# Performance work log

Measured on AMD Instinct MI355X. Metric: run time of the kernel, lower is better.

## Reference

```python
import jax, jax.numpy as jnp
import numpy as np

CH = 512
GROUPS = 32
EPS = 1e-5
B, H, W = 4, 64, 64


def setup_inputs() -> dict:
    key = jax.random.key(0)
    ks = jax.random.split(key, 6)
    s = 1.0 / np.sqrt(CH)  # conv2d default init scale (approx, uniform fan-in)
    return {
        "x": jax.random.normal(ks[0], (B, CH, H, W), dtype=jnp.float32),
        "norm_w": jnp.ones((CH,), jnp.float32),
        "norm_b": jnp.zeros((CH,), jnp.float32),
        "q_w": jax.random.normal(ks[1], (CH, CH), jnp.float32) * s,
        "q_b": jnp.zeros((CH,), jnp.float32),
        "k_w": jax.random.normal(ks[2], (CH, CH), jnp.float32) * s,
        "k_b": jnp.zeros((CH,), jnp.float32),
        "v_w": jax.random.normal(ks[3], (CH, CH), jnp.float32) * s,
        "v_b": jnp.zeros((CH,), jnp.float32),
        "proj_w": jax.random.normal(ks[4], (CH, CH), jnp.float32) * s,
        "proj_b": jnp.zeros((CH,), jnp.float32),
    }


def _group_norm(x, w, b):
    # x: [B, C, H, W]; 32 groups over channel dim
    bsz, c, h, wd = x.shape
    xg = x.reshape(bsz, GROUPS, c // GROUPS, h, wd)
    mean = xg.mean(axis=(2, 3, 4), keepdims=True)
    var = xg.var(axis=(2, 3, 4), keepdims=True)
    xg = (xg - mean) * jax.lax.rsqrt(var + EPS)
    x = xg.reshape(bsz, c, h, wd)
    return x * w[None, :, None, None] + b[None, :, None, None]


def _conv1x1(x, w, b):
    # x: [B, C, H, W], w: [O, C] -> [B, O, H, W]
    return jnp.einsum('bchw,oc->bohw', x, w) + b[None, :, None, None]


def reference(x, norm_w, norm_b, q_w, q_b, k_w, k_b, v_w, v_b, proj_w, proj_b):
    h = _group_norm(x, norm_w, norm_b)
    b, c, hh, ww = h.shape
    n = hh * ww
    q = _conv1x1(h, q_w, q_b).reshape(b, c, n).transpose(0, 2, 1)  # [b, n, c]
    k = _conv1x1(h, k_w, k_b).reshape(b, c, n)                     # [b, c, n]
    v = _conv1x1(h, v_w, v_b).reshape(b, c, n).transpose(0, 2, 1)  # [b, n, c]
    attn = jnp.einsum('bnc,bcm->bnm', q, k) * (c ** -0.5)          # [b, n, n]
    attn = jax.nn.softmax(attn, axis=-1)
    out = jnp.einsum('bnm,bmc->bnc', attn, v)                      # [b, n, c]
    out = out.transpose(0, 2, 1).reshape(b, c, hh, ww)
    return x + _conv1x1(out, proj_w, proj_b)
```

## Files before the change

kernel.cpp:

```cpp
#include <hip/hip_runtime.h>

#define NB 4
#define CH 512
#define NPIX 4096
#define GSZ 16
#define KVB 32
#define NT (NPIX / KVB)
#define DYN_LDS 136192
#define GEMM_LDS 65536

typedef __attribute__((ext_vector_type(8))) short bf16x8;
typedef __attribute__((ext_vector_type(4))) short bf16x4;
typedef __attribute__((ext_vector_type(4))) float f32x4;

#define MFMA __builtin_amdgcn_mfma_f32_16x16x32_bf16

static __device__ __forceinline__ short f2bf(float f) {
  unsigned u = __builtin_bit_cast(unsigned, f);
  u += 0x7fffu + ((u >> 16) & 1u);
  return (short)(u >> 16);
}

static __device__ __forceinline__ float bperm_f(int srclane, float v) {
  int r = __builtin_amdgcn_ds_bpermute(srclane << 2, __builtin_bit_cast(int, v));
  return __builtin_bit_cast(float, r);
}

typedef __attribute__((address_space(1))) unsigned glob_u32;
typedef __attribute__((address_space(3))) unsigned lds_u32;
static __device__ __forceinline__ void gl_lds16(const void* g, void* l) {
  __builtin_amdgcn_global_load_lds((const glob_u32*)g, (lds_u32*)l, 16, 0, 0);
}

__global__ __launch_bounds__(256) void wconv_kernel(
    const float* __restrict__ qw, const float* __restrict__ kw,
    const float* __restrict__ vw, const float* __restrict__ pw,
    short* __restrict__ wstack, short* __restrict__ wp) {
  int idx = (blockIdx.x * 256 + threadIdx.x) * 4;
  int mat = idx >> 18;
  int off = idx & 262143;
  const float* src = (mat == 0) ? qw : (mat == 1) ? kw : (mat == 2) ? vw : pw;
  short* dst = (mat < 3) ? (wstack + (size_t)mat * 262144) : wp;
  float4 v = *reinterpret_cast<const float4*>(src + off);
  bf16x4 o;
  o[0] = f2bf(v.x); o[1] = f2bf(v.y); o[2] = f2bf(v.z); o[3] = f2bf(v.w);
  *reinterpret_cast<bf16x4*>(dst + off) = o;
}

__global__ __launch_bounds__(256) void gn_stats_kernel(
    const float* __restrict__ x, float* __restrict__ st) {
  int b = blockIdx.x >> 5, g = blockIdx.x & 31;
  int tid = threadIdx.x;
  const float4* b4 = reinterpret_cast<const float4*>(
      x + (size_t)(b * CH + g * GSZ) * NPIX);
  float s = 0.f, s2 = 0.f;
  for (int i = tid; i < GSZ * NPIX / 4; i += 256) {
    float4 v = b4[i];
    s += v.x + v.y + v.z + v.w;
    s2 += v.x * v.x + v.y * v.y + v.z * v.z + v.w * v.w;
  }
  #pragma unroll
  for (int m = 1; m < 64; m <<= 1) { s += __shfl_xor(s, m); s2 += __shfl_xor(s2, m); }
  __shared__ float red[8];
  if ((tid & 63) == 0) { red[(tid >> 6) * 2] = s; red[(tid >> 6) * 2 + 1] = s2; }
  __syncthreads();
  if (tid == 0) {
    s = red[0] + red[2] + red[4] + red[6];
    s2 = red[1] + red[3] + red[5] + red[7];
    float mean = s * (1.f / 65536.f);
    float var = s2 * (1.f / 65536.f) - mean * mean;
    st[blockIdx.x * 2] = mean;
    st[blockIdx.x * 2 + 1] = rsqrtf(var + 1e-5f);
  }
}

__global__ __launch_bounds__(256) void gn_apply_kernel(
    const float* __restrict__ x, const float* __restrict__ nw,
    const float* __restrict__ nb, const float* __restrict__ st,
    short* __restrict__ hT) {
  int quarter = blockIdx.x & 3, pairid = blockIdx.x >> 2;
  int b = pairid >> 5, g = pairid & 31;
  int tid = threadIdx.x;
  float mean = st[pairid * 2], rstd = st[pairid * 2 + 1];
  int c = tid >> 4, nq = tid & 15;
  float wch = nw[g * GSZ + c] * rstd;
  float bch = nb[g * GSZ + c] - mean * wch;
  __shared__ short lt[GSZ][264];
  const float* base = x + (size_t)(b * CH + g * GSZ) * NPIX;
  short* outb = hT + (size_t)b * NPIX * CH + g * GSZ;
  const float* srcc = base + (size_t)c * NPIX + nq * 16;
  for (int chunk = quarter * 4; chunk < quarter * 4 + 4; ++chunk) {
    const float4* sp = reinterpret_cast<const float4*>(srcc + chunk * 256);
    float4 v0 = sp[0], v1 = sp[1], v2 = sp[2], v3 = sp[3];
    bf16x8 w0, w1;
    w0[0] = f2bf(v0.x * wch + bch); w0[1] = f2bf(v0.y * wch + bch);
    w0[2] = f2bf(v0.z * wch + bch); w0[3] = f2bf(v0.w * wch + bch);
    w0[4] = f2bf(v1.x * wch + bch); w0[5] = f2bf(v1.y * wch + bch);
    w0[6] = f2bf(v1.z * wch + bch); w0[7] = f2bf(v1.w * wch + bch);
    w1[0] = f2bf(v2.x * wch + bch); w1[1] = f2bf(v2.y * wch + bch);
    w1[2] = f2bf(v2.z * wch + bch); w1[3] = f2bf(v2.w * wch + bch);
    w1[4] = f2bf(v3.x * wch + bch); w1[5] = f2bf(v3.y * wch + bch);
    w1[6] = f2bf(v3.z * wch + bch); w1[7] = f2bf(v3.w * wch + bch);
    *reinterpret_cast<bf16x8*>(&lt[c][nq * 16]) = w0;
    *reinterpret_cast<bf16x8*>(&lt[c][nq * 16 + 8]) = w1;
    __syncthreads();
    bf16x8 o0, o1;
    #pragma unroll
    for (int cc = 0; cc < 8; ++cc) o0[cc] = lt[cc][tid];
    #pragma unroll
    for (int cc = 0; cc < 8; ++cc) o1[cc] = lt[cc + 8][tid];
    short* orow = outb + (size_t)(chunk * 256 + tid) * CH;
    *reinterpret_cast<bf16x8*>(orow) = o0;
    *reinterpret_cast<bf16x8*>(orow + 8) = o1;
    __syncthreads();
  }
}

__global__ __launch_bounds__(256) void qkv_kernel(
    const short* __restrict__ wstack, const short* __restrict__ hT,
    const float* __restrict__ qb, const float* __restrict__ kb,
    const float* __restrict__ vb,
    short* __restrict__ qT, short* __restrict__ kT, short* __restrict__ vC) {
  extern __shared__ char qsm[];
  char* abuf = qsm;
  char* bbuf = qsm + 32768;

  int hwid = blockIdx.x;
  int xcd = hwid & 7, slot = hwid >> 3;
  int by = slot % 12, gq = slot / 12;
  int grp = xcd + 8 * gq;
  int b = grp >> 5;
  int nbase = (grp & 31) * 128;
  int tid = threadIdx.x;
  int lane = tid & 63, wid = tid >> 6;
  int l15 = lane & 15, lg = lane >> 4;
  int wr = wid >> 1, wc = wid & 1;

  const short* arows = wstack + (size_t)by * 128 * CH;
  const short* brows = hT + ((size_t)b * NPIX + nbase) * CH;

  auto stage = [&](int buf, int kidx) {
    char* ad = abuf + buf * 16384;
    char* bd = bbuf + buf * 16384;
    #pragma unroll
    for (int i = 0; i < 4; ++i) {
      int off = i * 4096 + tid * 16;
      int row = off >> 7;
      int c16 = (off >> 4) & 7;
      int gchunk = (c16 ^ (row & 7)) * 8;
      gl_lds16(arows + (size_t)row * CH + kidx * 64 + gchunk, ad + off);
      gl_lds16(brows + (size_t)row * CH + kidx * 64 + gchunk, bd + off);
    }
  };

  f32x4 acc[4][4];
  #pragma unroll
  for (int mi = 0; mi < 4; ++mi)
    #pragma unroll
    for (int ni = 0; ni < 4; ++ni) acc[mi][ni] = (f32x4){0.f, 0.f, 0.f, 0.f};

  stage(0, 0);
  __syncthreads();

  int cur = 0;
  for (int kt = 0; kt < 8; ++kt) {
    if (kt + 1 < 8) stage(cur ^ 1, kt + 1);
    const char* ab = abuf + cur * 16384;
    const char* bb = bbuf + cur * 16384;
    #pragma unroll
    for (int ks = 0; ks < 2; ++ks) {
      bf16x8 af[4], bf[4];
      #pragma unroll
      for (int mi = 0; mi < 4; ++mi) {
        int row = wr * 64 + mi * 16 + l15;
        af[mi] = *reinterpret_cast<const bf16x8*>(
            ab + row * 128 + (((ks * 4 + lg) ^ (row & 7)) << 4));
      }
      #pragma unroll
      for (int ni = 0; ni < 4; ++ni) {
        int row = wc * 64 + ni * 16 + l15;
        bf[ni] = *reinterpret_cast<const bf16x8*>(
            bb + row * 128 + (((ks * 4 + lg) ^ (row & 7)) << 4));
      }
      #pragma unroll
      for (int mi = 0; mi < 4; ++mi)
        #pragma unroll
        for (int ni = 0; ni < 4; ++ni)
          acc[mi][ni] = MFMA(af[mi], bf[ni], acc[mi][ni], 0, 0, 0);
    }
    __syncthreads();
    cur ^= 1;
  }

  int oglob = by * 128;
  #pragma unroll
  for (int mi = 0; mi < 4; ++mi) {
    int oo = oglob + wr * 64 + mi * 16 + lg * 4;
    #pragma unroll
    for (int ni = 0; ni < 4; ++ni) {
      int nn = nbase + wc * 64 + ni * 16 + l15;
      f32x4 a = acc[mi][ni];
      if (oglob < 1024) {
        const float* bias = (oglob < 512) ? qb : kb;
        short* dstm = (oglob < 512) ? qT : kT;
        float sc = (oglob < 512) ? 0.044194173824159216f : 1.0f;
        int ol = oo & 511;
        bf16x4 pk;
        #pragma unroll
        for (int r = 0; r < 4; ++r) pk[r] = f2bf((a[r] + bias[ol + r]) * sc);
        *reinterpret_cast<bf16x4*>(dstm + ((size_t)b * NPIX + nn) * CH + ol) = pk;
      } else {
        int ov = oo - 1024;
        short* dstv = vC + ((size_t)b * CH + ov) * NPIX + nn;
        #pragma unroll
        for (int r = 0; r < 4; ++r) dstv[(size_t)r * NPIX] = f2bf(a[r] + vb[ov + r]);
      }
    }
  }
}

__global__ __launch_bounds__(512, 2) void flash_kernel(
    const short* __restrict__ qT, const short* __restrict__ kT,
    const short* __restrict__ vC, short* __restrict__ ao) {
  extern __shared__ char smem[];
  char* kbuf = smem;
  char* vbuf = smem + 65536;
  char* pbuf = smem + 131072;
  float* exch = (float*)(smem + 135168);

  int lin = blockIdx.y * 64 + blockIdx.x;
  int sw = (lin & 7) * 32 + (lin >> 3);
  int qb = sw & 63, b = sw >> 6;

  int tid = threadIdx.x;
  int lane = tid & 63, w = tid >> 6;
  int p = w >> 1, h = w & 1;
  int l15 = lane & 15, lg = lane >> 4;
  int qrow = qb * 64 + p * 16;

  const short* qptr = qT + ((size_t)b * NPIX + qrow + l15) * CH + lg * 8;
  bf16x8 qf[16];
  #pragma unroll
  for (int ks = 0; ks < 16; ++ks) qf[ks] = *reinterpret_cast<const bf16x8*>(qptr + ks * 32);

  f32x4 oacc[16];
  #pragma unroll
  for (int i = 0; i < 16; ++i) oacc[i] = (f32x4){0.f, 0.f, 0.f, 0.f};
  float mrow = -INFINITY, lrow = 0.f;
  bf16x8 pa_prev;
  bf16x8 vf_prev[16];
  #pragma unroll
  for (int i = 0; i < 8; ++i) pa_prev[i] = 0;
  #pragma unroll
  for (int j = 0; j < 16; ++j)
    #pragma unroll
    for (int i = 0; i < 8; ++i) vf_prev[j][i] = 0;

  const short* kTb = kT + (size_t)b * NPIX * CH;
  const short* vCb = vC + (size_t)b * CH * NPIX;
  const int swz = (l15 & 7) << 4;
  const int vswz = ((l15 >> 1) & 3) << 4;
  const int pswz = (l15 & 3) << 4;
  char* ppair = pbuf + p * 1024;
  float* exw = exch + (w * 16 + l15) * 2;
  float* exr = exch + ((w ^ 1) * 16 + l15) * 2;

  auto stage = [&](int buf, int t) {
    int m0 = t * KVB;
    char* kd = kbuf + buf * 32768;
    char* vd = vbuf + buf * 32768;
    #pragma unroll
    for (int i = 0; i < 4; ++i) {
      int r = w * 4 + i;
      const short* src = kTb + (size_t)(m0 + r) * CH + ((lane ^ (r & 7)) * 8);
      gl_lds16(src, kd + r * 1024);
    }
    #pragma unroll
    for (int i = 0; i < 4; ++i) {
      int j = w * 4 + i;
      int ch = j * 16 + (lane >> 2);
      const short* src = vCb + (size_t)ch * NPIX + m0 +
                         (((lane & 3) ^ ((lane >> 3) & 3)) * 8);
      gl_lds16(src, vd + j * 1024);
    }
  };

  stage(0, 0);
  asm volatile("s_waitcnt vmcnt(0)" ::: "memory");
  __syncthreads();

  int cur = 0;
  for (int t = 0; t < NT; ++t) {
    const char* kb_ = kbuf + cur * 32768;
    const char* vb_ = vbuf + cur * 32768;
    if (t + 1 < NT) stage(cur ^ 1, t + 1);
    f32x4 sa = (f32x4){0.f, 0.f, 0.f, 0.f};
    f32x4 sb = (f32x4){0.f, 0.f, 0.f, 0.f};
    __builtin_amdgcn_s_setprio(1);
    #pragma unroll
    for (int cs = 0; cs < 16; cs += 2) {
      bf16x8 kf0 = *reinterpret_cast<const bf16x8*>(
          kb_ + (h * 16 + l15) * 1024 + ((cs * 64 + lg * 16) ^ swz));
      bf16x8 kf1 = *reinterpret_cast<const bf16x8*>(
          kb_ + (h * 16 + l15) * 1024 + (((cs + 1) * 64 + lg * 16) ^ swz));
      sa = MFMA(kf0, qf[cs], sa, 0, 0, 0);
      sb = MFMA(kf1, qf[cs + 1], sb, 0, 0, 0);
    }
    __builtin_amdgcn_s_setprio(0);
    f32x4 st = sa + sb;
    float tmax = fmaxf(fmaxf(st[0], st[1]), fmaxf(st[2], st[3]));
    tmax = fmaxf(tmax, __shfl_xor(tmax, 16));
    tmax = fmaxf(tmax, __shfl_xor(tmax, 32));
    float pr[4];
    float psh;
    pr[0] = __expf(st[0] - tmax); pr[1] = __expf(st[1] - tmax);
    pr[2] = __expf(st[2] - tmax); pr[3] = __expf(st[3] - tmax);
    psh = (pr[0] + pr[1]) + (pr[2] + pr[3]);
    psh += __shfl_xor(psh, 16);
    psh += __shfl_xor(psh, 32);
    if (lane < 16) { exw[0] = tmax; exw[1] = psh; }
    asm volatile("s_waitcnt lgkmcnt(0)" ::: "memory");
    __builtin_amdgcn_s_barrier();
    __builtin_amdgcn_sched_barrier(0);
    float mo = exr[0], po = exr[1];
    float mnew = fmaxf(mrow, fmaxf(tmax, mo));
    float alpha = __expf(mrow - mnew);
    float scl = __expf(tmax - mnew);
    lrow = lrow * alpha + psh * scl + po * __expf(mo - mnew);
    mrow = mnew;
    {
      bf16x4 pk;
      pk[0] = f2bf(pr[0] * scl); pk[1] = f2bf(pr[1] * scl);
      pk[2] = f2bf(pr[2] * scl); pk[3] = f2bf(pr[3] * scl);
      *reinterpret_cast<bf16x4*>(ppair + l15 * 64 + ((h * 32 + lg * 8) ^ pswz)) = pk;
    }
    __builtin_amdgcn_s_setprio(1);
    #pragma unroll
    for (int j = 0; j < 16; ++j)
      oacc[j] = MFMA(pa_prev, vf_prev[j], oacc[j], 0, 0, 0);
    __builtin_amdgcn_s_setprio(0);
    if (!__all(alpha == 1.0f)) {
      float a4[4];
      #pragma unroll
      for (int r = 0; r < 4; ++r) a4[r] = bperm_f(lg * 4 + r, alpha);
      #pragma unroll
      for (int j = 0; j < 16; ++j) {
        oacc[j][0] *= a4[0]; oacc[j][1] *= a4[1];
        oacc[j][2] *= a4[2]; oacc[j][3] *= a4[3];
      }
    }
    #pragma unroll
    for (int j = 0; j < 16; ++j)
      vf_prev[j] = *reinterpret_cast<const bf16x8*>(
          vb_ + ((h * 16 + j) * 16 + l15) * 64 + ((lg * 16) ^ vswz));
    asm volatile("s_waitcnt vmcnt(0) lgkmcnt(0)" ::: "memory");
    __builtin_amdgcn_s_barrier();
    __builtin_amdgcn_sched_barrier(0);
    pa_prev = *reinterpret_cast<const bf16x8*>(ppair + l15 * 64 + ((lg * 16) ^ pswz));
    cur ^= 1;
  }
  #pragma unroll
  for (int j = 0; j < 16; ++j)
    oacc[j] = MFMA(pa_prev, vf_prev[j], oacc[j], 0, 0, 0);

  float linv = 1.f / lrow;
  float r4[4];
  #pragma unroll
  for (int r = 0; r < 4; ++r) r4[r] = bperm_f(lg * 4 + r, linv);
  short* aob = ao + ((size_t)b * NPIX + qrow) * CH;
  #pragma unroll
  for (int j = 0; j < 16; ++j) {
    int cb2 = h * 16 + j;
    #pragma unroll
    for (int r = 0; r < 4; ++r) {
      aob[(size_t)(lg * 4 + r) * CH + cb2 * 16 + l15] = f2bf(oacc[j][r] * r4[r]);
    }
  }
}

__global__ __launch_bounds__(256) void proj_kernel(
    const short* __restrict__ wpm, const short* __restrict__ ao,
    const float* __restrict__ x, const float* __restrict__ pb,
    float* __restrict__ out) {
  extern __shared__ char qsm[];
  char* abuf = qsm;
  char* bbuf = qsm + 32768;

  int hwid = blockIdx.x;
  int xcd = hwid & 7, slot = hwid >> 3;
  int by = slot & 3, gq = slot >> 2;
  int grp = xcd + 8 * gq;
  int b = grp >> 5;
  int nbase = (grp & 31) * 128;
  int tid = threadIdx.x;
  int lane = tid & 63, wid = tid >> 6;
  int l15 = lane & 15, lg = lane >> 4;
  int wr = wid >> 1, wc = wid & 1;

  const short* arows = wpm + (size_t)by * 128 * CH;
  const short* brows = ao + ((size_t)b * NPIX + nbase) * CH;

  auto stage = [&](int buf, int kidx) {
    char* ad = abuf + buf * 16384;
    char* bd = bbuf + buf * 16384;
    #pragma unroll
    for (int i = 0; i < 4; ++i) {
      int off = i * 4096 + tid * 16;
      int row = off >> 7;
      int c16 = (off >> 4) & 7;
      int gchunk = (c16 ^ (row & 7)) * 8;
      gl_lds16(arows + (size_t)row * CH + kidx * 64 + gchunk, ad + off);
      gl_lds16(brows + (size_t)row * CH + kidx * 64 + gchunk, bd + off);
    }
  };

  f32x4 acc[4][4];
  #pragma unroll
  for (int mi = 0; mi < 4; ++mi)
    #pragma unroll
    for (int ni = 0; ni < 4; ++ni) acc[mi][ni] = (f32x4){0.f, 0.f, 0.f, 0.f};

  stage(0, 0);
  __syncthreads();

  int cur = 0;
  for (int kt = 0; kt < 8; ++kt) {
    if (kt + 1 < 8) stage(cur ^ 1, kt + 1);
    const char* ab = abuf + cur * 16384;
    const char* bb = bbuf + cur * 16384;
    #pragma unroll
    for (int ks = 0; ks < 2; ++ks) {
      bf16x8 af[4], bf[4];
      #pragma unroll
      for (int mi = 0; mi < 4; ++mi) {
        int row = wr * 64 + mi * 16 + l15;
        af[mi] = *reinterpret_cast<const bf16x8*>(
            ab + row * 128 + (((ks * 4 + lg) ^ (row & 7)) << 4));
      }
      #pragma unroll
      for (int ni = 0; ni < 4; ++ni) {
        int row = wc * 64 + ni * 16 + l15;
        bf[ni] = *reinterpret_cast<const bf16x8*>(
            bb + row * 128 + (((ks * 4 + lg) ^ (row & 7)) << 4));
      }
      #pragma unroll
      for (int mi = 0; mi < 4; ++mi)
        #pragma unroll
        for (int ni = 0; ni < 4; ++ni)
          acc[mi][ni] = MFMA(af[mi], bf[ni], acc[mi][ni], 0, 0, 0);
    }
    __syncthreads();
    cur ^= 1;
  }

  #pragma unroll
  for (int mi = 0; mi < 4; ++mi) {
    int oo = by * 128 + wr * 64 + mi * 16 + lg * 4;
    #pragma unroll
    for (int ni = 0; ni < 4; ++ni) {
      int nn = nbase + wc * 64 + ni * 16 + l15;
      f32x4 a = acc[mi][ni];
      #pragma unroll
      for (int r = 0; r < 4; ++r) {
        size_t idx = ((size_t)b * CH + oo + r) * NPIX + nn;
        out[idx] = a[r] + pb[oo + r] + x[idx];
      }
    }
  }
}

extern "C" void kernel_launch(void* const* d_in, const int* in_sizes, int n_in,
                              void* d_out, int out_size, void* d_ws, size_t ws_size,
                              hipStream_t stream) {
  const float* x  = (const float*)d_in[0];
  const float* nw = (const float*)d_in[1];
  const float* nb = (const float*)d_in[2];
  const float* qw = (const float*)d_in[3];
  const float* qb = (const float*)d_in[4];
  const float* kw = (const float*)d_in[5];
  const float* kb = (const float*)d_in[6];
  const float* vw = (const float*)d_in[7];
  const float* vb = (const float*)d_in[8];
  const float* pw = (const float*)d_in[9];
  const float* pb = (const float*)d_in[10];
  char* ws = (char*)d_ws;
  short* wstack = (short*)(ws);
  short* wp     = (short*)(ws + 1572864);
  float* gnstat = (float*)(ws + 2097152);
  short* hT     = (short*)(ws + 2101248);
  short* qT     = (short*)(ws + 18878464);
  short* kT     = (short*)(ws + 35655680);
  short* vC     = (short*)(ws + 52432896);
  short* ao     = hT;
  float* out = (float*)d_out;

  hipFuncSetAttribute((const void*)flash_kernel,
                      hipFuncAttributeMaxDynamicSharedMemorySize, DYN_LDS);
  hipFuncSetAttribute((const void*)qkv_kernel,
                      hipFuncAttributeMaxDynamicSharedMemorySize, GEMM_LDS);
  hipFuncSetAttribute((const void*)proj_kernel,
                      hipFuncAttributeMaxDynamicSharedMemorySize, GEMM_LDS);

  wconv_kernel<<<1024, 256, 0, stream>>>(qw, kw, vw, pw, wstack, wp);
  gn_stats_kernel<<<128, 256, 0, stream>>>(x, gnstat);
  gn_apply_kernel<<<512, 256, 0, stream>>>(x, nw, nb, gnstat, hT);
  qkv_kernel<<<1536, 256, GEMM_LDS, stream>>>(wstack, hT, qb, kb, vb, qT, kT, vC);
  flash_kernel<<<dim3(64, NB), 512, DYN_LDS, stream>>>(qT, kT, vC, ao);
  proj_kernel<<<512, 256, GEMM_LDS, stream>>>(wp, ao, x, pb, out);
}
```

Baseline: 435.2 us.

## Double-buffer softmax stats exchange to drop one barrier per KV tile

The two half-waves that split each KV tile now write their row max, row sum and unscaled bf16 probabilities into alternating LDS slots. The cross-half merge of softmax statistics, the rescale of the output accumulators and the rescale of P all move after the existing end-of-iteration barrier. This removes the separate mid-iteration barrier and LDS wait that used to sit between the QK^T and PV phases. In exchange, P is rounded to bf16 twice, slightly reducing precision, and LDS use grows a little.

```diff
diff --git a/kernel.cpp b/kernel.cpp
--- a/kernel.cpp
+++ b/kernel.cpp
@@ -6,7 +6,7 @@
 #define GSZ 16
 #define KVB 32
 #define NT (NPIX / KVB)
-#define DYN_LDS 136192
+#define DYN_LDS 141312
 #define GEMM_LDS 65536
 
 typedef __attribute__((ext_vector_type(8))) short bf16x8;
@@ -19,6 +19,11 @@
   unsigned u = __builtin_bit_cast(unsigned, f);
   u += 0x7fffu + ((u >> 16) & 1u);
   return (short)(u >> 16);
+}
+
+static __device__ __forceinline__ float bf2f(short s) {
+  unsigned u = ((unsigned)(unsigned short)s) << 16;
+  return __builtin_bit_cast(float, u);
 }
 
 static __device__ __forceinline__ float bperm_f(int srclane, float v) {
@@ -226,7 +231,7 @@
   char* kbuf = smem;
   char* vbuf = smem + 65536;
   char* pbuf = smem + 131072;
-  float* exch = (float*)(smem + 135168);
+  float* exch = (float*)(smem + 139264);
 
   int lin = blockIdx.y * 64 + blockIdx.x;
   int sw = (lin & 7) * 32 + (lin >> 3);
@@ -293,6 +298,7 @@
   for (int t = 0; t < NT; ++t) {
     const char* kb_ = kbuf + cur * 32768;
     const char* vb_ = vbuf + cur * 32768;
+    int slot = t & 1;
     if (t + 1 < NT) stage(cur ^ 1, t + 1);
     f32x4 sa = (f32x4){0.f, 0.f, 0.f, 0.f};
     f32x4 sb = (f32x4){0.f, 0.f, 0.f, 0.f};
@@ -318,37 +324,19 @@
     psh = (pr[0] + pr[1]) + (pr[2] + pr[3]);
     psh += __shfl_xor(psh, 16);
     psh += __shfl_xor(psh, 32);
-    if (lane < 16) { exw[0] = tmax; exw[1] = psh; }
-    asm volatile("s_waitcnt lgkmcnt(0)" ::: "memory");
-    __builtin_amdgcn_s_barrier();
-    __builtin_amdgcn_sched_barrier(0);
-    float mo = exr[0], po = exr[1];
-    float mnew = fmaxf(mrow, fmaxf(tmax, mo));
-    float alpha = __expf(mrow - mnew);
-    float scl = __expf(tmax - mnew);
-    lrow = lrow * alpha + psh * scl + po * __expf(mo - mnew);
-    mrow = mnew;
+    if (lane < 16) { exw[slot * 256] = tmax; exw[slot * 256 + 1] = psh; }
     {
       bf16x4 pk;
-      pk[0] = f2bf(pr[0] * scl); pk[1] = f2bf(pr[1] * scl);
-      pk[2] = f2bf(pr[2] * scl); pk[3] = f2bf(pr[3] * scl);
-      *reinterpret_cast<bf16x4*>(ppair + l15 * 64 + ((h * 32 + lg * 8) ^ pswz)) = pk;
+      pk[0] = f2bf(pr[0]); pk[1] = f2bf(pr[1]);
+      pk[2] = f2bf(pr[2]); pk[3] = f2bf(pr[3]);
+      *reinterpret_cast<bf16x4*>(ppair + slot * 4096 + l15 * 64 +
+                                 ((h * 32 + lg * 8) ^ pswz)) = pk;
     }
     __builtin_amdgcn_s_setprio(1);
     #pragma unroll
     for (int j = 0; j < 16; ++j)
       oacc[j] = MFMA(pa_prev, vf_prev[j], oacc[j], 0, 0, 0);
     __builtin_amdgcn_s_setprio(0);
-    if (!__all(alpha == 1.0f)) {
-      float a4[4];
-      #pragma unroll
-      for (int r = 0; r < 4; ++r) a4[r] = bperm_f(lg * 4 + r, alpha);
-      #pragma unroll
-      for (int j = 0; j < 16; ++j) {
-        oacc[j][0] *= a4[0]; oacc[j][1] *= a4[1];
-        oacc[j][2] *= a4[2]; oacc[j][3] *= a4[3];
-      }
-    }
     #pragma unroll
     for (int j = 0; j < 16; ++j)
       vf_prev[j] = *reinterpret_cast<const bf16x8*>(
@@ -356,7 +344,33 @@
     asm volatile("s_waitcnt vmcnt(0) lgkmcnt(0)" ::: "memory");
     __builtin_amdgcn_s_barrier();
     __builtin_amdgcn_sched_barrier(0);
-    pa_prev = *reinterpret_cast<const bf16x8*>(ppair + l15 * 64 + ((lg * 16) ^ pswz));
+    float mo = exr[slot * 256], po = exr[slot * 256 + 1];
+    float mnew = fmaxf(mrow, fmaxf(tmax, mo));
+    float alpha = __expf(mrow - mnew);
+    float scl_own = __expf(tmax - mnew);
+    float scl_oth = __expf(mo - mnew);
+    lrow = lrow * alpha + psh * scl_own + po * scl_oth;
+    mrow = mnew;
+    if (!__all(alpha == 1.0f)) {
+      float a4[4];
+      #pragma unroll
+      for (int r = 0; r < 4; ++r) a4[r] = bperm_f(lg * 4 + r, alpha);
+      #pragma unroll
+      for (int j = 0; j < 16; ++j) {
+        oacc[j][0] *= a4[0]; oacc[j][1] *= a4[1];
+        oacc[j][2] *= a4[2]; oacc[j][3] *= a4[3];
+      }
+    }
+    {
+      bf16x8 praw = *reinterpret_cast<const bf16x8*>(
+          ppair + slot * 4096 + l15 * 64 + ((lg * 16) ^ pswz));
+      float scl_h0 = (h == 0) ? scl_own : scl_oth;
+      float scl_h1 = (h == 0) ? scl_oth : scl_own;
+      float s_lane = (lg < 2) ? scl_h0 : scl_h1;
+      #pragma unroll
+      for (int i = 0; i < 8; ++i)
+        pa_prev[i] = f2bf(bf2f(praw[i]) * s_lane);
+    }
     cur ^= 1;
   }
   #pragma unroll
```

Result: slower. 512.5 us (+17.7%).
